# Kernel tuning notes

Measured on AMD Instinct MI355X. Metric: run time of the kernel, lower is better.

Reference implementation:

```python
import jax, jax.numpy as jnp
import numpy as np

V = 32000; DM = 512; DS = 64; K = 4; INNER = 2048; KK = 3
B = 4; N = 512; LOOPS = 6; H_CYCLES = 2; POWER = 2


def _ln(x, g, b, eps=1e-5):
    mu = jnp.mean(x, -1, keepdims=True)
    var = jnp.mean(jnp.square(x - mu), -1, keepdims=True)
    return (x - mu) * jax.lax.rsqrt(var + eps) * g + b


def _sn(W, u):
    # torch spectral_norm: one power iteration (no grad through u,v), sigma differentiable through W
    v = W.T @ u
    v = v / (jnp.linalg.norm(v) + 1e-12)
    u2 = W @ v
    u2 = u2 / (jnp.linalg.norm(u2) + 1e-12)
    u2 = jax.lax.stop_gradient(u2)
    v = jax.lax.stop_gradient(v)
    sigma = u2 @ (W @ v)
    return W / sigma


def _block(Q_in, p):
    Qn = _ln(Q_in, p['g1'], p['b1'])                       # [B,N,d]
    qp = Qn.mean(1)                                        # [B,d]
    Wq = _sn(p['hqW'], p['uq'])
    Wk = _sn(p['hkW'], p['uk'])
    Oq = (qp @ Wq.T).reshape(-1, DM, DS)                   # [B,d,D]
    Ok = (qp @ Wk.T).reshape(-1, DM, DS)
    Pq = jax.nn.elu(jnp.einsum('bnd,bde->bne', Qn, Oq) + p['BQ']) + 1.0
    Pk = jax.nn.elu(jnp.einsum('bnd,bde->bne', Qn, Ok) + p['BK']) + 1.0
    Wm = jnp.maximum(jnp.einsum('bne,bme->bnm', Pq, Pk), 0.0) ** POWER  # [B,N,N]
    Att = jnp.einsum('bnm,bmd->bnd', Wm, Qn)
    Nrm = jnp.abs(Wm.sum(-1)) + 1.0                        # [B,N]
    m = Att / Nrm[..., None] - Qn
    mp = m @ p['mW'].T + p['mb']
    Qi = Q_in + jax.nn.softplus(p['dt']) * mp
    Qn2 = _ln(Qi, p['g2'], p['b2'])
    GU = Qn2 @ p['WupW'].T                                 # [B,N,2*inner]
    G, U = GU[..., :INNER], GU[..., INNER:]
    H = jax.nn.silu(G) * U
    Ht = jnp.transpose(H, (0, 2, 1))                       # [B,inner,N]
    Hc = jax.lax.conv_general_dilated(Ht, p['convW'], (1,), [(1, 1)],
                                      dimension_numbers=('NCH', 'OIH', 'NCH'),
                                      feature_group_count=INNER)
    Hc = jnp.transpose(Hc, (0, 2, 1))
    return Qi + Hc @ p['WdownW'].T


def _run(Q, bp):
    for i in range(K):
        Q = _block(Q, {k: v[i] for k, v in bp.items()})
    return Q


def setup_inputs() -> dict:
    key = jax.random.key(0)
    ks = iter(jax.random.split(key, 48))
    nrm = lambda s, std=0.02: jax.random.normal(next(ks), s, jnp.float32) * std
    inp = {}
    inp['inputs'] = jax.random.randint(next(ks), (B, N), 0, V, jnp.int32)
    inp['labels'] = jax.random.randint(next(ks), (B, N), 0, V, jnp.int32)
    inp['halted'] = jnp.ones((B,), bool)
    inp['steps'] = jnp.zeros((B,), jnp.int32)
    inp['carry_hidden'] = jnp.zeros((B, N, DM), jnp.float32)
    inp['carry_inputs'] = jnp.zeros((B, N), jnp.int32)
    inp['carry_labels'] = jnp.zeros((B, N), jnp.int32)
    inp['embedding'] = nrm((V, DM))
    inp['pos_emb'] = nrm((8192, DM))
    inp['in_g'] = jnp.ones((DM,), jnp.float32)
    inp['in_b'] = jnp.zeros((DM,), jnp.float32)
    inp['init_hidden'] = nrm((DM,))
    inp['dt'] = jnp.full((K,), 0.1, jnp.float32)
    inp['mW'] = nrm((K, DM, DM))
    inp['mb'] = jnp.zeros((K, DM), jnp.float32)
    inp['hqW'] = nrm((K, DM * DS, DM))
    inp['hkW'] = nrm((K, DM * DS, DM))
    uq = jax.random.normal(next(ks), (K, DM * DS), jnp.float32)
    uk = jax.random.normal(next(ks), (K, DM * DS), jnp.float32)
    inp['uq'] = uq / jnp.linalg.norm(uq, axis=-1, keepdims=True)
    inp['uk'] = uk / jnp.linalg.norm(uk, axis=-1, keepdims=True)
    inp['BQ'] = nrm((K, DS))
    inp['BK'] = nrm((K, DS))
    inp['g1'] = jnp.ones((K, DM), jnp.float32)
    inp['b1'] = jnp.zeros((K, DM), jnp.float32)
    inp['g2'] = jnp.ones((K, DM), jnp.float32)
    inp['b2'] = jnp.zeros((K, DM), jnp.float32)
    inp['WupW'] = nrm((K, 2 * INNER, DM))
    inp['convW'] = nrm((K, INNER, 1, KK))
    inp['WdownW'] = nrm((K, DM, INNER))
    inp['fin_g'] = jnp.ones((DM,), jnp.float32)
    inp['fin_b'] = jnp.zeros((DM,), jnp.float32)
    inp['halt_W'] = nrm((1, DM))
    inp['halt_b'] = jnp.full((1,), -5.0, jnp.float32)
    inp['lm_head'] = nrm((V, DM))
    return inp


def reference(inputs, labels, halted, steps, carry_hidden, carry_inputs, carry_labels,
              embedding, pos_emb, in_g, in_b, init_hidden, dt, mW, mb, hqW, hkW, uq, uk,
              BQ, BK, g1, b1, g2, b2, WupW, convW, WdownW, fin_g, fin_b, halt_W, halt_b, lm_head):
    bp = dict(dt=dt, mW=mW, mb=mb, hqW=hqW, hkW=hkW, uq=uq, uk=uk, BQ=BQ, BK=BK,
              g1=g1, b1=b1, g2=g2, b2=b2, WupW=WupW, convW=convW, WdownW=WdownW)
    new_hidden = jnp.where(halted[:, None, None], init_hidden, carry_hidden)
    new_steps = jnp.where(halted, jnp.zeros_like(steps), steps)
    new_inputs = jnp.where(halted[:, None], inputs, carry_inputs)
    X = _ln(embedding[new_inputs] + pos_emb[:inputs.shape[1]][None], in_g, in_b)
    Q = new_hidden
    for _ in range(H_CYCLES - 1):  # no_grad burn-in
        Q = jax.lax.stop_gradient(_run(Q + X, bp))
    Q = _run(Q + X, bp)            # gradient pass (L_cycles = 1)
    Qf = _ln(Q, fin_g, fin_b)
    logits = Qf @ lm_head.T
    halt_logits = Qf.mean(1) @ halt_W.T + halt_b
    new_steps = new_steps + 1
    new_halted = new_steps >= LOOPS
    return logits, halt_logits, jax.lax.stop_gradient(Q), new_steps, new_halted
```

## Files before the change

### kernel.cpp

```cpp
#include <hip/hip_runtime.h>
#include <stdint.h>

#define DMD 512
#define NSEQ 512
#define NBATCH 4
#define WROWS 32768
#define VOCAB 32000

#define OFF_HALT   65536000L
#define OFF_Q      65536004L
#define OFF_STEPS  66584580L
#define OFF_HALTED 66584584L

typedef __attribute__((ext_vector_type(8))) short short8v;
typedef __attribute__((ext_vector_type(4))) float f32x4;

__device__ __forceinline__ ushort f2bf(float f){
  uint u = __builtin_bit_cast(uint, f);
  u += 0x7fffu + ((u >> 16) & 1u);
  return (ushort)(u >> 16);
}
__device__ __forceinline__ float bf2f(ushort h){
  return __builtin_bit_cast(float, (uint)h << 16);
}

__device__ __forceinline__ float block_reduce_sum256(float v, float* red){
  int t = threadIdx.x;
  red[t] = v; __syncthreads();
  for (int o = 128; o; o >>= 1){
    if (t < o) red[t] += red[t+o];
    __syncthreads();
  }
  float r = red[0]; __syncthreads();
  return r;
}

template<int MODE, int TR, int QP, int HALT>
__global__ __launch_bounds__(512) void k_ln1(
    const float* in, float* QaW, const float* X,
    const int* halted32, const float* ih, const float* ch,
    ushort* __restrict__ outb, ushort* __restrict__ outT,
    float* __restrict__ qp_part,
    const float* __restrict__ g, const float* __restrict__ b,
    const float* __restrict__ hW, float* __restrict__ hpart)
{
  __shared__ ushort lt[TR ? 16 : 1][TR ? 520 : 1];
  __shared__ float red[QP ? 4096 : 1];
  const int bb = blockIdx.y, rg = blockIdx.x;
  const int n0 = rg*16;
  const int tid = threadIdx.x, wave = tid >> 6, lane = tid & 63;
  const int c8 = lane*8;
  float qacc[8] = {};
  #pragma unroll
  for (int rr = 0; rr < 2; rr++){
    const int n = n0 + wave*2 + rr;
    const long rowo = (long)bb*262144 + (long)n*512;
    float x[8];
    if (MODE == 1){
      bool hall = (halted32[0] != 0);
      #pragma unroll
      for (int i = 0; i < 8; i++){
        float base = hall ? ih[c8+i] : ch[rowo + c8 + i];
        x[i] = base + X[rowo + c8 + i];
      }
      #pragma unroll
      for (int i = 0; i < 8; i++) QaW[rowo + c8 + i] = x[i];
    } else if (MODE == 2){
      #pragma unroll
      for (int i = 0; i < 8; i++) x[i] = in[rowo + c8 + i] + X[rowo + c8 + i];
      #pragma unroll
      for (int i = 0; i < 8; i++) QaW[rowo + c8 + i] = x[i];
    } else {
      float4 a0 = *(const float4*)(in + rowo + c8);
      float4 a1 = *(const float4*)(in + rowo + c8 + 4);
      x[0]=a0.x; x[1]=a0.y; x[2]=a0.z; x[3]=a0.w;
      x[4]=a1.x; x[5]=a1.y; x[6]=a1.z; x[7]=a1.w;
    }
    float s = 0.f, sq = 0.f;
    #pragma unroll
    for (int i = 0; i < 8; i++){ s += x[i]; sq += x[i]*x[i]; }
    #pragma unroll
    for (int m = 32; m; m >>= 1){
      s  += __shfl_xor(s, m);
      sq += __shfl_xor(sq, m);
    }
    float mu = s*(1.f/512.f);
    float var = sq*(1.f/512.f) - mu*mu;
    float rs = rsqrtf(var + 1e-5f);
    float hd = 0.f;
    short8v ov;
    #pragma unroll
    for (int i = 0; i < 8; i++){
      float o = (x[i]-mu)*rs*g[c8+i] + b[c8+i];
      ov[i] = (short)f2bf(o);
      if (QP) qacc[i] += o;
      if (HALT) hd += o * hW[c8+i];
    }
    *(short8v*)&outb[rowo + c8] = ov;
    if (TR) *(short8v*)&lt[n & 15][c8] = ov;
    if (HALT){
      #pragma unroll
      for (int m = 32; m; m >>= 1) hd += __shfl_xor(hd, m);
      if (lane == 0) atomicAdd(&hpart[bb], hd);
    }
  }
  if (QP){
    #pragma unroll
    for (int i = 0; i < 8; i++) red[wave*512 + c8 + i] = qacc[i];
    __syncthreads();
    if (wave == 0){
      #pragma unroll
      for (int i = 0; i < 8; i++){
        int c = c8 + i;
        float s = 0.f;
        #pragma unroll
        for (int w = 0; w < 8; w++) s += red[w*512 + c];
        qp_part[((long)bb*32 + rg)*512 + c] = s;
      }
    }
  }
  if (TR){
    __syncthreads();
    #pragma unroll 4
    for (int p = 0; p < 16; p++){
      int d = p*32 + (tid >> 4);
      int n = tid & 15;
      outT[(long)bb*262144 + (long)d*512 + n0 + n] = lt[n][d];
    }
  }
}

__global__ void k_embed_ln(const int* __restrict__ inputs, const int* __restrict__ cinputs,
                           const int* __restrict__ halted32,
                           const float* __restrict__ emb, const float* __restrict__ pos,
                           const float* __restrict__ g, const float* __restrict__ b,
                           float* __restrict__ X){
  __shared__ float red[256];
  int r = blockIdx.x; int t = threadIdx.x;
  int n = r & 511;
  bool hall = (halted32[0] != 0);
  int tok = hall ? inputs[r] : cinputs[r];
  const float* e = emb + (long)tok*DMD;
  const float* p = pos + (long)n*DMD;
  float v0 = e[t]+p[t], v1 = e[t+256]+p[t+256];
  float mu = block_reduce_sum256(v0+v1, red) * (1.f/DMD);
  float d0 = v0-mu, d1 = v1-mu;
  float var = block_reduce_sum256(d0*d0+d1*d1, red) * (1.f/DMD);
  float rs = rsqrtf(var + 1e-5f);
  X[(long)r*DMD+t]     = d0*rs*g[t]     + b[t];
  X[(long)r*DMD+t+256] = d1*rs*g[t+256] + b[t+256];
}

__global__ __launch_bounds__(512) void k_sn_v(
    const float* __restrict__ hqW, const float* __restrict__ hkW,
    const float* __restrict__ uq, const float* __restrict__ uk,
    float* __restrict__ vpart, ushort* __restrict__ Wbf){
  __shared__ float red[8*520];
  int z = blockIdx.y; int k = z >> 1, qk = z & 1;
  const float* W = (qk ? hkW : hqW) + (long)k*WROWS*DMD;
  const float* u = (qk ? uk : uq) + (long)k*WROWS;
  ushort* Wb = Wbf ? (Wbf + (long)z*WROWS*DMD) : nullptr;
  int t = threadIdx.x;
  int c8 = (t & 63) * 8;
  int rsub = t >> 6;
  int r0 = blockIdx.x * 256;
  float acc[8] = {};
  for (int r = rsub; r < 256; r += 16){
    int ra = r0 + r, rb = r0 + r + 8;
    long offa = (long)ra*DMD + c8, offb = (long)rb*DMD + c8;
    float4 a0 = *(const float4*)(W + offa);
    float4 a1 = *(const float4*)(W + offa + 4);
    float4 b0 = *(const float4*)(W + offb);
    float4 b1 = *(const float4*)(W + offb + 4);
    float ua = u[ra], ub = u[rb];
    float av[8] = {a0.x,a0.y,a0.z,a0.w,a1.x,a1.y,a1.z,a1.w};
    float bv[8] = {b0.x,b0.y,b0.z,b0.w,b1.x,b1.y,b1.z,b1.w};
    #pragma unroll
    for (int i = 0; i < 8; i++) acc[i] += av[i]*ua + bv[i]*ub;
    if (Wb){
      short8v oa, ob;
      #pragma unroll
      for (int i = 0; i < 8; i++){ oa[i] = (short)f2bf(av[i]); ob[i] = (short)f2bf(bv[i]); }
      long ca = (long)((ra & 63)*512 + (ra >> 6));
      long cb = (long)((rb & 63)*512 + (rb >> 6));
      *(short8v*)(Wb + ca*DMD + c8) = oa;
      *(short8v*)(Wb + cb*DMD + c8) = ob;
    }
  }
  #pragma unroll
  for (int i = 0; i < 8; i++) red[rsub*520 + c8 + i] = acc[i];
  __syncthreads();
  if (rsub == 0){
    #pragma unroll
    for (int i = 0; i < 8; i++){
      int c = c8 + i;
      float s = 0.f;
      #pragma unroll
      for (int w = 0; w < 8; w++) s += red[w*520 + c];
      vpart[((long)z*128 + blockIdx.x)*512 + c] = s;
    }
  }
}

__global__ __launch_bounds__(512) void k_sn_norm(const float* __restrict__ vpart,
                                                 float* __restrict__ vraw,
                                                 ushort* __restrict__ qpb){
  __shared__ float red[512];
  int z = blockIdx.x; int t = threadIdx.x;
  float s = 0.f;
  for (int c = 0; c < 128; c++) s += vpart[((long)z*128 + c)*512 + t];
  red[t] = s*s; __syncthreads();
  for (int o = 256; o; o >>= 1){
    if (t < o) red[t] += red[t+o];
    __syncthreads();
  }
  float nrm = sqrtf(red[0]);
  float v = s / (nrm + 1e-12f);
  vraw[z*512 + t] = v;
  ushort* p = qpb + (long)z*32768;
  p[4*512 + t] = f2bf(v);
  for (int r = 5; r < 64; r++) p[r*512 + t] = 0;
}

__global__ void k_sn_s(const float* __restrict__ hqW, const float* __restrict__ hkW,
                       const float* __restrict__ vraw, float* __restrict__ ssqp){
  int z = blockIdx.y; int k = z >> 1, qk = z & 1;
  const float* W = (qk ? hkW : hqW) + (long)k*WROWS*DMD;
  const float* v = vraw + z*DMD;
  int wave = threadIdx.x >> 6, lane = threadIdx.x & 63;
  float vreg[8];
  #pragma unroll
  for (int i = 0; i < 8; i++) vreg[i] = v[lane + 64*i];
  int r0 = blockIdx.x*256 + wave*64;
  float acc = 0.f;
  for (int r = r0; r < r0+64; r++){
    float p = 0.f;
    #pragma unroll
    for (int i = 0; i < 8; i++)
      p += W[(long)r*DMD + lane + 64*i] * vreg[i];
    for (int off = 32; off; off >>= 1) p += __shfl_down(p, off);
    if (lane == 0) acc += p*p;
  }
  if (lane == 0) atomicAdd(&ssqp[z*64 + (blockIdx.x & 63)], acc);
}

__global__ void k_proj(const float* __restrict__ hqW, const float* __restrict__ hkW,
                       const float* __restrict__ qp,
                       ushort* __restrict__ OqT, ushort* __restrict__ OkT, int k){
  int z = blockIdx.y;
  const float* W = (z ? hkW : hqW) + (long)k*WROWS*DMD;
  ushort* O = z ? OkT : OqT;
  int wave = threadIdx.x >> 6, lane = threadIdx.x & 63;
  long r = (long)blockIdx.x*4 + wave;
  float a0=0,a1=0,a2=0,a3=0;
  for (int j = lane; j < DMD; j += 64){
    float w = W[r*DMD + j];
    a0 += w*qp[j]; a1 += w*qp[DMD+j]; a2 += w*qp[2*DMD+j]; a3 += w*qp[3*DMD+j];
  }
  for (int off = 32; off; off >>= 1){
    a0 += __shfl_down(a0,off); a1 += __shfl_down(a1,off);
    a2 += __shfl_down(a2,off); a3 += __shfl_down(a3,off);
  }
  if (lane == 0){
    int d = (int)(r >> 6), e = (int)(r & 63);
    long o = (long)e*512 + d;
    O[o] = f2bf(a0); O[32768+o] = f2bf(a1);
    O[2*32768+o] = f2bf(a2); O[3*32768+o] = f2bf(a3);
  }
}

template<int BM, int BN, int WM, int WN, int EPI, int BFOUT, int DUAL, int RSUM>
__global__ __launch_bounds__(256) void mm_bt(
    const ushort* __restrict__ A, const ushort* __restrict__ B, void* __restrict__ C,
    int N, int K, long sA, long sB, long sC,
    const float* __restrict__ bias, const float* __restrict__ bias2,
    const float* __restrict__ res, const ushort* __restrict__ resb,
    const float* __restrict__ dtp, int dtidx,
    float* __restrict__ aux, const float* __restrict__ ssqp)
{
  __shared__ ushort As[BM*64];
  __shared__ ushort Bs[BN*64];
  const int z = blockIdx.z;
  const float* biasz = bias;
  if (DUAL){
    A += (long)(z & 3)*sA;
    if (z >= 4) biasz = bias2;
  } else {
    A += (long)z*sA;
  }
  B += (long)z*sB;
  const int tm = blockIdx.y*BM, tn = DUAL ? 0 : blockIdx.x*BN;
  const int tid = threadIdx.x;
  const int wid = tid >> 6, lane = tid & 63;
  constexpr int NWN = BN/WN;
  const int wr = wid / NWN, wc = wid % NWN;
  constexpr int FM = WM/16, FN = WN/16;
  const int ln15 = lane & 15, kq = lane >> 4;
  constexpr int LA = BM/32;
  constexpr int LB = BN/32;
  f32x4 acc[FM][FN] = {};

  for (int k0 = 0; k0 < K; k0 += 64){
    #pragma unroll
    for (int l = 0; l < LA; l++){
      int slot = tid + l*256;
      int row = slot >> 3, ch = slot & 7;
      int gch = ch ^ (row & 7);
      const char* g = (const char*)(A + (long)(tm+row)*K + k0) + gch*16;
      ushort* lp = As + (size_t)(wid*64 + l*256)*8;
      __builtin_amdgcn_global_load_lds((const __attribute__((address_space(1))) void*)g,
                                       (__attribute__((address_space(3))) void*)lp, 16, 0, 0);
    }
    #pragma unroll
    for (int l = 0; l < LB; l++){
      int slot = tid + l*256;
      int row = slot >> 3, ch = slot & 7;
      int gch = ch ^ (row & 7);
      const char* g = (const char*)(B + (long)(tn+row)*K + k0) + gch*16;
      ushort* lp = Bs + (size_t)(wid*64 + l*256)*8;
      __builtin_amdgcn_global_load_lds((const __attribute__((address_space(1))) void*)g,
                                       (__attribute__((address_space(3))) void*)lp, 16, 0, 0);
    }
    __syncthreads();
    #pragma unroll
    for (int ks = 0; ks < 2; ks++){
      short8v af[FM], bfr[FN];
      #pragma unroll
      for (int i = 0; i < FM; i++){
        int row = wr*WM + i*16 + ln15;
        af[i] = *(const short8v*)&As[row*64 + (((ks*4+kq) ^ (row&7))*8)];
      }
      #pragma unroll
      for (int j = 0; j < FN; j++){
        int row = wc*WN + j*16 + ln15;
        bfr[j] = *(const short8v*)&Bs[row*64 + (((ks*4+kq) ^ (row&7))*8)];
      }
      #pragma unroll
      for (int i = 0; i < FM; i++)
        #pragma unroll
        for (int j = 0; j < FN; j++)
          acc[i][j] = __builtin_amdgcn_mfma_f32_16x16x32_bf16(af[i], bfr[j], acc[i][j], 0, 0, 0);
    }
    __syncthreads();
  }

  float sp = 0.f, invs = 1.f;
  if (EPI == 3) sp = log1pf(expf(dtp[dtidx]));
  if (EPI == 1){
    const float* sq = ssqp + (DUAL ? (z >> 2)*64 : 0);
    float s2 = 0.f;
    for (int i = 0; i < 64; i++) s2 += sq[i];
    invs = (sqrtf(s2) + 1e-12f) / s2;
  }
  float* Cf = (float*)C + (long)z*sC;
  ushort* Cb = (ushort*)C + (long)z*sC;
  const float* rz = res ? (res + (long)z*sC) : nullptr;
  const ushort* rzb = resb ? (resb + (long)z*sC) : nullptr;
  const float* nrmz = (EPI == 5) ? (bias + (long)z*512) : nullptr;
  float rsv[FM][4] = {};
  float sacc = 0.f;
  #pragma unroll
  for (int i = 0; i < FM; i++){
    int row0 = tm + wr*WM + i*16 + kq*4;
    #pragma unroll
    for (int j = 0; j < FN; j++){
      int col = tn + wc*WN + j*16 + ln15;
      #pragma unroll
      for (int r = 0; r < 4; r++){
        int row = row0 + r;
        long idx = (long)row*N + col;
        float v = acc[i][j][r];
        if (EPI == 6){
          if (row < 4) Cb[idx] = f2bf(v);
          else if (row == 4) sacc += v*v;
          continue;
        }
        if (EPI == 1){ v = v*invs + biasz[col]; v = v > 0.f ? v : expm1f(v); v += 1.f; }
        else if (EPI == 2){ v = fmaxf(v, 0.f); v = v*v; if (RSUM) rsv[i][r] += v; }
        else if (EPI == 3){ v = rz[idx] + sp*(v + biasz[col]); }
        else if (EPI == 4){ v = v + rz[idx]; if (aux) aux[idx] = v; }
        else if (EPI == 5){ v = v/(fabsf(nrmz[row])+1.f) - bf2f(rzb[idx]); }
        if (BFOUT) Cb[idx] = f2bf(v);
        else       Cf[idx] = v;
      }
    }
  }
  if (EPI == 6){
    if (aux){
      sacc += __shfl_xor(sacc, 1); sacc += __shfl_xor(sacc, 2);
      sacc += __shfl_xor(sacc, 4); sacc += __shfl_xor(sacc, 8);
      if (wr == 0 && kq == 1 && ln15 == 0)
        atomicAdd(&aux[(long)z*64 + ((int)blockIdx.x & 63)], sacc);
    }
    return;
  }
  if (RSUM && EPI == 2){
    #pragma unroll
    for (int i = 0; i < FM; i++){
      #pragma unroll
      for (int r = 0; r < 4; r++){
        float x = rsv[i][r];
        x += __shfl_xor(x, 1); x += __shfl_xor(x, 2);
        x += __shfl_xor(x, 4); x += __shfl_xor(x, 8);
        if (ln15 == 0)
          atomicAdd(&aux[(long)z*512 + tm + wr*WM + i*16 + kq*4 + r], x);
      }
    }
  }
}

__global__ void k_qp2(const float* __restrict__ part, float* __restrict__ qp,
                      ushort* __restrict__ qpb, float* __restrict__ nrm_raw){
  int b = blockIdx.x, t = threadIdx.x;
  float s = 0.f;
  #pragma unroll
  for (int c = 0; c < 32; c++) s += part[((long)b*32 + c)*512 + t];
  float val = s * (1.f/512.f);
  qp[b*512 + t] = val;
  ushort bv = f2bf(val);
  #pragma unroll
  for (int z = 0; z < 8; z++)
    qpb[(long)z*32768 + (long)b*512 + t] = bv;
  nrm_raw[b*512 + t] = 0.f;
}

__global__ void k_convfuse(const ushort* __restrict__ GU, const float* __restrict__ w,
                           ushort* __restrict__ Hc){
  int r = blockIdx.x;
  int n = r & 511;
  int c = threadIdx.x * 8;
  long base = (long)r*4096 + c;
  float o[8] = {};
  if (n > 0){
    short8v gv = *(const short8v*)&GU[base-4096];
    short8v uv = *(const short8v*)&GU[base-4096+2048];
    #pragma unroll
    for (int i = 0; i < 8; i++){
      float g = bf2f((ushort)gv[i]), u = bf2f((ushort)uv[i]);
      o[i] += g/(1.f+expf(-g))*u * w[(c+i)*3+0];
    }
  }
  {
    short8v gv = *(const short8v*)&GU[base];
    short8v uv = *(const short8v*)&GU[base+2048];
    #pragma unroll
    for (int i = 0; i < 8; i++){
      float g = bf2f((ushort)gv[i]), u = bf2f((ushort)uv[i]);
      o[i] += g/(1.f+expf(-g))*u * w[(c+i)*3+1];
    }
  }
  if (n < 511){
    short8v gv = *(const short8v*)&GU[base+4096];
    short8v uv = *(const short8v*)&GU[base+4096+2048];
    #pragma unroll
    for (int i = 0; i < 8; i++){
      float g = bf2f((ushort)gv[i]), u = bf2f((ushort)uv[i]);
      o[i] += g/(1.f+expf(-g))*u * w[(c+i)*3+2];
    }
  }
  short8v ov;
  #pragma unroll
  for (int i = 0; i < 8; i++) ov[i] = (short)f2bf(o[i]);
  *(short8v*)&Hc[(long)r*2048 + c] = ov;
}

__global__ void k_cvt3(const float* __restrict__ s0, ushort* __restrict__ d0, long n0,
                       const float* __restrict__ s1, ushort* __restrict__ d1, long n1,
                       const float* __restrict__ s2, ushort* __restrict__ d2, long n2){
  long i = ((long)blockIdx.x*256 + threadIdx.x)*4;
  const float* s; ushort* d; long off;
  if (i < n0){ s = s0; d = d0; off = i; }
  else if (i < n0 + n1){ s = s1; d = d1; off = i - n0; }
  else { s = s2; d = d2; off = i - n0 - n1; }
  float4 v = *(const float4*)(s + off);
  ushort4 o;
  o.x = f2bf(v.x); o.y = f2bf(v.y); o.z = f2bf(v.z); o.w = f2bf(v.w);
  *(ushort4*)(d + off) = o;
}

__global__ void k_cvt(const float* __restrict__ in, ushort* __restrict__ out){
  long i = ((long)blockIdx.x*256 + threadIdx.x)*4;
  float4 v = *(const float4*)(in + i);
  ushort4 o;
  o.x = f2bf(v.x); o.y = f2bf(v.y); o.z = f2bf(v.z); o.w = f2bf(v.w);
  *(ushort4*)(out + i) = o;
}

__global__ void k_fin(const int* __restrict__ halted32, const int* __restrict__ steps,
                      const float* __restrict__ hpart, const float* __restrict__ hb,
                      float* __restrict__ o_halt, float* __restrict__ o_steps,
                      float* __restrict__ o_halted){
  int t = threadIdx.x;
  if (t < NBATCH){
    o_halt[t] = hpart[t]*(1.f/512.f) + hb[0];
    bool hall = (halted32[0] != 0);
    int ns = (hall ? 0 : steps[t]) + 1;
    o_steps[t] = (float)ns;
    o_halted[t] = ns >= 6 ? 1.f : 0.f;
  }
}

extern "C" void kernel_launch(void* const* d_in, const int* in_sizes, int n_in,
                              void* d_out, int out_size, void* d_ws, size_t ws_size,
                              hipStream_t stream)
{
  const int*     inputs       = (const int*)d_in[0];
  const int*     halted32     = (const int*)d_in[2];
  const int*     steps        = (const int*)d_in[3];
  const float*   carry_hidden = (const float*)d_in[4];
  const int*     carry_inputs = (const int*)d_in[5];
  const float*   embedding    = (const float*)d_in[7];
  const float*   pos_emb      = (const float*)d_in[8];
  const float*   in_g = (const float*)d_in[9];
  const float*   in_b = (const float*)d_in[10];
  const float*   init_hidden = (const float*)d_in[11];
  const float*   dt   = (const float*)d_in[12];
  const float*   mW   = (const float*)d_in[13];
  const float*   mb   = (const float*)d_in[14];
  const float*   hqW  = (const float*)d_in[15];
  const float*   hkW  = (const float*)d_in[16];
  const float*   uq   = (const float*)d_in[17];
  const float*   uk   = (const float*)d_in[18];
  const float*   BQb  = (const float*)d_in[19];
  const float*   BKb  = (const float*)d_in[20];
  const float*   g1   = (const float*)d_in[21];
  const float*   b1   = (const float*)d_in[22];
  const float*   g2   = (const float*)d_in[23];
  const float*   b2   = (const float*)d_in[24];
  const float*   WupW = (const float*)d_in[25];
  const float*   convW= (const float*)d_in[26];
  const float*   WdownW=(const float*)d_in[27];
  const float*   fin_g= (const float*)d_in[28];
  const float*   fin_b= (const float*)d_in[29];
  const float*   halt_W=(const float*)d_in[30];
  const float*   halt_b=(const float*)d_in[31];
  const float*   lm_head=(const float*)d_in[32];
  float* out = (float*)d_out;

  float* ws = (float*)d_ws;
  float*  X    = ws;
  float*  Qa   = ws +  1048576;
  float*  Qb   = ws +  2097152;
  ushort* qpb  = (ushort*)(ws + 3145728);
  float*  vpart  = ws + 3276800;
  float*  qp_part= ws + 3801088;
  ushort* GU_bf  = (ushort*)(ws +  4194304);
  ushort* Hc_bf  = (ushort*)(ws +  8388608);
  ushort* m_bf   = (ushort*)(ws + 10485760);
  ushort* Wm_bf  = (ushort*)(ws + 11010048);
  ushort* QnT_bf = (ushort*)(ws + 11534336);
  ushort* Pq_bf  = (ushort*)(ws + 12058624);
  ushort* OqT    = (ushort*)(ws + 12189696);
  ushort* lm_bf  = (ushort*)(ws +  4194304);
  ushort* Qn_bf  = (ushort*)(ws + 13369344);
  ushort* mW_bf  = (ushort*)(ws + 13893632);
  ushort* Wup_bf = (ushort*)(ws + 14417920);
  ushort* Wdn_bf = (ushort*)(ws + 18612224);
  float*  qp       = ws + 20709376;
  float*  Nrm_raw  = ws + 20711424;
  float*  vraw     = ws + 20713472;
  float*  ssq_part = ws + 20717568;
  float*  hpart    = ws + 20718080;
  ushort* W_bf = (ushort*)(ws + 20750976);
  const size_t NEED_BF = (size_t)(20750976 + 67108864) * 4;
  const bool useBf = ws_size >= NEED_BF;

  k_cvt3<<<13312, 256, 0, stream>>>(mW, mW_bf, 1048576L,
                                    WupW, Wup_bf, 8388608L,
                                    WdownW, Wdn_bf, 4194304L);

  hipMemsetAsync(ssq_part, 0, 576*sizeof(float), stream);
  k_sn_v<<<dim3(128,8), 512, 0, stream>>>(hqW, hkW, uq, uk, vpart,
                                          useBf ? W_bf : nullptr);
  k_sn_norm<<<8, 512, 0, stream>>>(vpart, vraw, qpb);
  if (!useBf)
    k_sn_s<<<dim3(128,8), 256, 0, stream>>>(hqW, hkW, vraw, ssq_part);

  k_embed_ln<<<2048, 256, 0, stream>>>(inputs, carry_inputs, halted32,
                                       embedding, pos_emb, in_g, in_b, X);

  for (int cyc = 0; cyc < 2; cyc++){
    for (int k = 0; k < 4; k++){
      if (k == 0){
        if (cyc == 0)
          k_ln1<1,1,1,0><<<dim3(32,4), 512, 0, stream>>>(
              Qa, Qa, X, halted32, init_hidden, carry_hidden,
              Qn_bf, QnT_bf, qp_part, g1 + k*DMD, b1 + k*DMD, nullptr, nullptr);
        else
          k_ln1<2,1,1,0><<<dim3(32,4), 512, 0, stream>>>(
              Qa, Qa, X, nullptr, nullptr, nullptr,
              Qn_bf, QnT_bf, qp_part, g1 + k*DMD, b1 + k*DMD, nullptr, nullptr);
      } else {
        k_ln1<0,1,1,0><<<dim3(32,4), 512, 0, stream>>>(
            Qa, nullptr, nullptr, nullptr, nullptr, nullptr,
            Qn_bf, QnT_bf, qp_part, g1 + k*DMD, b1 + k*DMD, nullptr, nullptr);
      }
      k_qp2<<<4, 512, 0, stream>>>(qp_part, qp, qpb, Nrm_raw);
      if (useBf)
        mm_bt<64,64,32,32,6,1,0,1><<<dim3(512,1,2), 256, 0, stream>>>(
            qpb + (long)k*2*32768, W_bf + (long)k*2*16777216, OqT,
            32768, 512, 32768, 16777216, 131072,
            nullptr, nullptr, nullptr, nullptr, nullptr, 0,
            (cyc == 0) ? (ssq_part + k*128) : nullptr, nullptr);
      else
        k_proj<<<dim3(8192,2), 256, 0, stream>>>(hqW, hkW, qp, OqT, OqT + 131072, k);
      mm_bt<64,64,32,32,1,1,1,0><<<dim3(1,8,8), 256, 0, stream>>>(
          Qn_bf, OqT, Pq_bf, 64, 512, 262144, 32768, 32768,
          BQb + k*64, BKb + k*64, nullptr, nullptr, nullptr, 0,
          nullptr, ssq_part + k*128);
      mm_bt<64,64,32,32,2,1,0,1><<<dim3(8,8,4), 256, 0, stream>>>(
          Pq_bf, Pq_bf + 131072, Wm_bf, 512, 64, 32768, 32768, 262144,
          nullptr, nullptr, nullptr, nullptr, nullptr, 0, Nrm_raw, nullptr);
      mm_bt<64,64,32,32,5,1,0,0><<<dim3(8,8,4), 256, 0, stream>>>(
          Wm_bf, QnT_bf, m_bf, 512, 512, 262144, 262144, 262144,
          Nrm_raw, nullptr, nullptr, Qn_bf, nullptr, 0, nullptr, nullptr);
      mm_bt<64,64,32,32,3,0,0,0><<<dim3(8,32,1), 256, 0, stream>>>(
          m_bf, mW_bf + (long)k*262144, Qb, 512, 512, 0, 0, 0,
          mb + k*DMD, nullptr, Qa, nullptr, dt, k, nullptr, nullptr);
      k_ln1<0,0,0,0><<<dim3(32,4), 512, 0, stream>>>(
          Qb, nullptr, nullptr, nullptr, nullptr, nullptr,
          Qn_bf, nullptr, nullptr, g2 + k*DMD, b2 + k*DMD, nullptr, nullptr);
      mm_bt<128,128,64,64,0,1,0,0><<<dim3(32,16,1), 256, 0, stream>>>(
          Qn_bf, Wup_bf + (long)k*2097152, GU_bf, 4096, 512, 0, 0, 0,
          nullptr, nullptr, nullptr, nullptr, nullptr, 0, nullptr, nullptr);
      k_convfuse<<<2048, 256, 0, stream>>>(GU_bf, convW + (long)k*2048*3, Hc_bf);
      float* aux = (cyc == 1 && k == 3) ? (out + OFF_Q) : nullptr;
      mm_bt<64,64,32,32,4,0,0,0><<<dim3(8,32,1), 256, 0, stream>>>(
          Hc_bf, Wdn_bf + (long)k*1048576, Qa, 512, 2048, 0, 0, 0,
          nullptr, nullptr, Qb, nullptr, nullptr, 0, aux, nullptr);
    }
  }

  k_ln1<0,0,0,1><<<dim3(32,4), 512, 0, stream>>>(
      Qa, nullptr, nullptr, nullptr, nullptr, nullptr,
      Qn_bf, nullptr, nullptr, fin_g, fin_b, halt_W, hpart);
  k_cvt<<<16000, 256, 0, stream>>>(lm_head, lm_bf);
  mm_bt<128,128,64,64,0,0,0,0><<<dim3(250,16,1), 256, 0, stream>>>(
      Qn_bf, lm_bf, out, 32000, 512, 0, 0, 0,
      nullptr, nullptr, nullptr, nullptr, nullptr, 0, nullptr, nullptr);
  k_fin<<<1, 64, 0, stream>>>(halted32, steps, hpart, halt_b,
                              out + OFF_HALT, out + OFF_STEPS, out + OFF_HALTED);
}
```

Before: 1.546 ms.

## Fuse attention score and value matmuls; convert lm_head to bf16 inside GEMM loads

Adds a k_attn kernel that computes the squared-ReLU scores Pq·Pkᵀ tile by tile in LDS, accumulates the row normalizers locally, and immediately multiplies each score tile by Qn. This removes the [B,N,N] Wm buffer round-trip, the Nrm atomics and their zeroing, and one launch per block. Separately, the lm_head GEMM now reads fp32 weights and converts them to bf16 while staging into LDS, replacing the standalone k_cvt pass. The attention kernel recomputes scores once per 64-column output group (8 groups), and the fused conversion gives up the async global_load_lds path for B.

```diff
diff --git a/kernel.cpp b/kernel.cpp
--- a/kernel.cpp
+++ b/kernel.cpp
@@ -269,7 +269,7 @@
   }
 }
 
-template<int BM, int BN, int WM, int WN, int EPI, int BFOUT, int DUAL, int RSUM>
+template<int BM, int BN, int WM, int WN, int EPI, int BFOUT, int DUAL, int RSUM, int CVTB = 0>
 __global__ __launch_bounds__(256) void mm_bt(
     const ushort* __restrict__ A, const ushort* __restrict__ B, void* __restrict__ C,
     int N, int K, long sA, long sB, long sC,
@@ -288,7 +288,7 @@
   } else {
     A += (long)z*sA;
   }
-  B += (long)z*sB;
+  if (!CVTB) B += (long)z*sB;
   const int tm = blockIdx.y*BM, tn = DUAL ? 0 : blockIdx.x*BN;
   const int tid = threadIdx.x;
   const int wid = tid >> 6, lane = tid & 63;
@@ -316,10 +316,22 @@
       int slot = tid + l*256;
       int row = slot >> 3, ch = slot & 7;
       int gch = ch ^ (row & 7);
-      const char* g = (const char*)(B + (long)(tn+row)*K + k0) + gch*16;
-      ushort* lp = Bs + (size_t)(wid*64 + l*256)*8;
-      __builtin_amdgcn_global_load_lds((const __attribute__((address_space(1))) void*)g,
-                                       (__attribute__((address_space(3))) void*)lp, 16, 0, 0);
+      if (CVTB){
+        const float* Bf = (const float*)B;
+        const float* src = Bf + (long)(tn+row)*K + k0 + gch*8;
+        float4 v0 = *(const float4*)src;
+        float4 v1 = *(const float4*)(src + 4);
+        float vv[8] = {v0.x,v0.y,v0.z,v0.w,v1.x,v1.y,v1.z,v1.w};
+        short8v o;
+        #pragma unroll
+        for (int i = 0; i < 8; i++) o[i] = (short)f2bf(vv[i]);
+        *(short8v*)&Bs[(size_t)slot*8] = o;
+      } else {
+        const char* g = (const char*)(B + (long)(tn+row)*K + k0) + gch*16;
+        ushort* lp = Bs + (size_t)(wid*64 + l*256)*8;
+        __builtin_amdgcn_global_load_lds((const __attribute__((address_space(1))) void*)g,
+                                         (__attribute__((address_space(3))) void*)lp, 16, 0, 0);
+      }
     }
     __syncthreads();
     #pragma unroll
@@ -355,9 +367,6 @@
   float* Cf = (float*)C + (long)z*sC;
   ushort* Cb = (ushort*)C + (long)z*sC;
   const float* rz = res ? (res + (long)z*sC) : nullptr;
-  const ushort* rzb = resb ? (resb + (long)z*sC) : nullptr;
-  const float* nrmz = (EPI == 5) ? (bias + (long)z*512) : nullptr;
-  float rsv[FM][4] = {};
   float sacc = 0.f;
   #pragma unroll
   for (int i = 0; i < FM; i++){
@@ -376,41 +385,152 @@
           continue;
         }
         if (EPI == 1){ v = v*invs + biasz[col]; v = v > 0.f ? v : expm1f(v); v += 1.f; }
-        else if (EPI == 2){ v = fmaxf(v, 0.f); v = v*v; if (RSUM) rsv[i][r] += v; }
         else if (EPI == 3){ v = rz[idx] + sp*(v + biasz[col]); }
         else if (EPI == 4){ v = v + rz[idx]; if (aux) aux[idx] = v; }
-        else if (EPI == 5){ v = v/(fabsf(nrmz[row])+1.f) - bf2f(rzb[idx]); }
         if (BFOUT) Cb[idx] = f2bf(v);
         else       Cf[idx] = v;
       }
     }
   }
-  if (EPI == 6){
-    if (aux){
-      sacc += __shfl_xor(sacc, 1); sacc += __shfl_xor(sacc, 2);
-      sacc += __shfl_xor(sacc, 4); sacc += __shfl_xor(sacc, 8);
-      if (wr == 0 && kq == 1 && ln15 == 0)
-        atomicAdd(&aux[(long)z*64 + ((int)blockIdx.x & 63)], sacc);
-    }
-    return;
-  }
-  if (RSUM && EPI == 2){
-    #pragma unroll
-    for (int i = 0; i < FM; i++){
+  if (EPI == 6 && aux){
+    sacc += __shfl_xor(sacc, 1); sacc += __shfl_xor(sacc, 2);
+    sacc += __shfl_xor(sacc, 4); sacc += __shfl_xor(sacc, 8);
+    if (wr == 0 && kq == 1 && ln15 == 0)
+      atomicAdd(&aux[(long)z*64 + ((int)blockIdx.x & 63)], sacc);
+  }
+}
+
+__global__ __launch_bounds__(256) void k_attn(
+    const ushort* __restrict__ Pqk, const ushort* __restrict__ QnT,
+    const ushort* __restrict__ Qn, ushort* __restrict__ m_out)
+{
+  __shared__ ushort Aq[64*64];
+  __shared__ ushort Bk[64*64];
+  __shared__ ushort Qs[64*64];
+  __shared__ ushort Ws[64*72];
+  __shared__ float nrmL[2][64];
+  const int cg = blockIdx.x, nt = blockIdx.y, b = blockIdx.z;
+  const int tid = threadIdx.x, wid = tid >> 6;
+  const int lane = tid & 63, ln15 = lane & 15, kq = lane >> 4;
+  const int wr = wid >> 1, wc = wid & 1;
+  const ushort* Pq  = Pqk + (long)b*32768 + (long)nt*4096;
+  const ushort* Pk0 = Pqk + 131072 + (long)b*32768;
+  const ushort* Qt  = QnT + (long)b*262144 + (long)(cg*64)*512;
+
+  #pragma unroll
+  for (int l = 0; l < 2; l++){
+    int slot = tid + l*256;
+    int row = slot >> 3, gch = (slot & 7) ^ (row & 7);
+    __builtin_amdgcn_global_load_lds(
+        (const __attribute__((address_space(1))) void*)((const char*)(Pq + (long)row*64) + gch*16),
+        (__attribute__((address_space(3))) void*)(Aq + (size_t)(wid*64 + l*256)*8), 16, 0, 0);
+  }
+  f32x4 acc[2][2] = {};
+  float nacc[2][4] = {};
+  for (int mt = 0; mt < 8; mt++){
+    #pragma unroll
+    for (int l = 0; l < 2; l++){
+      int slot = tid + l*256;
+      int row = slot >> 3, gch = (slot & 7) ^ (row & 7);
+      __builtin_amdgcn_global_load_lds(
+          (const __attribute__((address_space(1))) void*)((const char*)(Pk0 + (long)mt*4096 + (long)row*64) + gch*16),
+          (__attribute__((address_space(3))) void*)(Bk + (size_t)(wid*64 + l*256)*8), 16, 0, 0);
+      __builtin_amdgcn_global_load_lds(
+          (const __attribute__((address_space(1))) void*)((const char*)(Qt + (long)row*512 + mt*64) + gch*16),
+          (__attribute__((address_space(3))) void*)(Qs + (size_t)(wid*64 + l*256)*8), 16, 0, 0);
+    }
+    __syncthreads();
+    f32x4 sA[2][2] = {};
+    #pragma unroll
+    for (int ks = 0; ks < 2; ks++){
+      short8v af[2], bfr[2];
+      #pragma unroll
+      for (int i = 0; i < 2; i++){
+        int row = wr*32 + i*16 + ln15;
+        af[i] = *(const short8v*)&Aq[row*64 + (((ks*4+kq) ^ (row&7))*8)];
+      }
+      #pragma unroll
+      for (int j = 0; j < 2; j++){
+        int row = wc*32 + j*16 + ln15;
+        bfr[j] = *(const short8v*)&Bk[row*64 + (((ks*4+kq) ^ (row&7))*8)];
+      }
+      #pragma unroll
+      for (int i = 0; i < 2; i++)
+        #pragma unroll
+        for (int j = 0; j < 2; j++)
+          sA[i][j] = __builtin_amdgcn_mfma_f32_16x16x32_bf16(af[i], bfr[j], sA[i][j], 0, 0, 0);
+    }
+    float t[2][4] = {};
+    #pragma unroll
+    for (int i = 0; i < 2; i++)
+      #pragma unroll
+      for (int j = 0; j < 2; j++)
+        #pragma unroll
+        for (int r = 0; r < 4; r++){
+          float v = fmaxf(sA[i][j][r], 0.f); v = v*v;
+          t[i][r] += v;
+          int row = wr*32 + i*16 + kq*4 + r;
+          int col = wc*32 + j*16 + ln15;
+          Ws[row*72 + col] = f2bf(v);
+        }
+    #pragma unroll
+    for (int i = 0; i < 2; i++)
       #pragma unroll
       for (int r = 0; r < 4; r++){
-        float x = rsv[i][r];
+        float x = t[i][r];
         x += __shfl_xor(x, 1); x += __shfl_xor(x, 2);
         x += __shfl_xor(x, 4); x += __shfl_xor(x, 8);
-        if (ln15 == 0)
-          atomicAdd(&aux[(long)z*512 + tm + wr*WM + i*16 + kq*4 + r], x);
+        nacc[i][r] += x;
+      }
+    __syncthreads();
+    #pragma unroll
+    for (int ks = 0; ks < 2; ks++){
+      short8v af[2], bfr[2];
+      #pragma unroll
+      for (int i = 0; i < 2; i++){
+        int row = wr*32 + i*16 + ln15;
+        af[i] = *(const short8v*)&Ws[row*72 + (ks*4+kq)*8];
+      }
+      #pragma unroll
+      for (int j = 0; j < 2; j++){
+        int row = wc*32 + j*16 + ln15;
+        bfr[j] = *(const short8v*)&Qs[row*64 + (((ks*4+kq) ^ (row&7))*8)];
+      }
+      #pragma unroll
+      for (int i = 0; i < 2; i++)
+        #pragma unroll
+        for (int j = 0; j < 2; j++)
+          acc[i][j] = __builtin_amdgcn_mfma_f32_16x16x32_bf16(af[i], bfr[j], acc[i][j], 0, 0, 0);
+    }
+    __syncthreads();
+  }
+  if (ln15 == 0){
+    #pragma unroll
+    for (int i = 0; i < 2; i++)
+      #pragma unroll
+      for (int r = 0; r < 4; r++)
+        nrmL[wc][wr*32 + i*16 + kq*4 + r] = nacc[i][r];
+  }
+  __syncthreads();
+  #pragma unroll
+  for (int i = 0; i < 2; i++){
+    #pragma unroll
+    for (int r = 0; r < 4; r++){
+      int rowl = wr*32 + i*16 + kq*4 + r;
+      float Nr = fabsf(nrmL[0][rowl] + nrmL[1][rowl]) + 1.f;
+      int n = nt*64 + rowl;
+      #pragma unroll
+      for (int j = 0; j < 2; j++){
+        int col = cg*64 + wc*32 + j*16 + ln15;
+        long idx = (long)b*262144 + (long)n*512 + col;
+        m_out[idx] = f2bf(acc[i][j][r]/Nr - bf2f(Qn[idx]));
       }
     }
   }
 }
 
 __global__ void k_qp2(const float* __restrict__ part, float* __restrict__ qp,
-                      ushort* __restrict__ qpb, float* __restrict__ nrm_raw){
+                      ushort* __restrict__ qpb){
   int b = blockIdx.x, t = threadIdx.x;
   float s = 0.f;
   #pragma unroll
@@ -421,7 +541,6 @@
   #pragma unroll
   for (int z = 0; z < 8; z++)
     qpb[(long)z*32768 + (long)b*512 + t] = bv;
-  nrm_raw[b*512 + t] = 0.f;
 }
 
 __global__ void k_convfuse(const ushort* __restrict__ GU, const float* __restrict__ w,
@@ -476,14 +595,6 @@
   ushort4 o;
   o.x = f2bf(v.x); o.y = f2bf(v.y); o.z = f2bf(v.z); o.w = f2bf(v.w);
   *(ushort4*)(d + off) = o;
-}
-
-__global__ void k_cvt(const float* __restrict__ in, ushort* __restrict__ out){
-  long i = ((long)blockIdx.x*256 + threadIdx.x)*4;
-  float4 v = *(const float4*)(in + i);
-  ushort4 o;
-  o.x = f2bf(v.x); o.y = f2bf(v.y); o.z = f2bf(v.z); o.w = f2bf(v.w);
-  *(ushort4*)(out + i) = o;
 }
 
 __global__ void k_fin(const int* __restrict__ halted32, const int* __restrict__ steps,
@@ -547,17 +658,14 @@
   ushort* GU_bf  = (ushort*)(ws +  4194304);
   ushort* Hc_bf  = (ushort*)(ws +  8388608);
   ushort* m_bf   = (ushort*)(ws + 10485760);
-  ushort* Wm_bf  = (ushort*)(ws + 11010048);
   ushort* QnT_bf = (ushort*)(ws + 11534336);
   ushort* Pq_bf  = (ushort*)(ws + 12058624);
   ushort* OqT    = (ushort*)(ws + 12189696);
-  ushort* lm_bf  = (ushort*)(ws +  4194304);
   ushort* Qn_bf  = (ushort*)(ws + 13369344);
   ushort* mW_bf  = (ushort*)(ws + 13893632);
   ushort* Wup_bf = (ushort*)(ws + 14417920);
   ushort* Wdn_bf = (ushort*)(ws + 18612224);
   float*  qp       = ws + 20709376;
-  float*  Nrm_raw  = ws + 20711424;
   float*  vraw     = ws + 20713472;
   float*  ssq_part = ws + 20717568;
   float*  hpart    = ws + 20718080;
@@ -595,7 +703,7 @@
             Qa, nullptr, nullptr, nullptr, nullptr, nullptr,
             Qn_bf, QnT_bf, qp_part, g1 + k*DMD, b1 + k*DMD, nullptr, nullptr);
       }
-      k_qp2<<<4, 512, 0, stream>>>(qp_part, qp, qpb, Nrm_raw);
+      k_qp2<<<4, 512, 0, stream>>>(qp_part, qp, qpb);
       if (useBf)
         mm_bt<64,64,32,32,6,1,0,1><<<dim3(512,1,2), 256, 0, stream>>>(
             qpb + (long)k*2*32768, W_bf + (long)k*2*16777216, OqT,
@@ -608,12 +716,7 @@
           Qn_bf, OqT, Pq_bf, 64, 512, 262144, 32768, 32768,
           BQb + k*64, BKb + k*64, nullptr, nullptr, nullptr, 0,
           nullptr, ssq_part + k*128);
-      mm_bt<64,64,32,32,2,1,0,1><<<dim3(8,8,4), 256, 0, stream>>>(
-          Pq_bf, Pq_bf + 131072, Wm_bf, 512, 64, 32768, 32768, 262144,
-          nullptr, nullptr, nullptr, nullptr, nullptr, 0, Nrm_raw, nullptr);
-      mm_bt<64,64,32,32,5,1,0,0><<<dim3(8,8,4), 256, 0, stream>>>(
-          Wm_bf, QnT_bf, m_bf, 512, 512, 262144, 262144, 262144,
-          Nrm_raw, nullptr, nullptr, Qn_bf, nullptr, 0, nullptr, nullptr);
+      k_attn<<<dim3(8,8,4), 256, 0, stream>>>(Pq_bf, QnT_bf, Qn_bf, m_bf);
       mm_bt<64,64,32,32,3,0,0,0><<<dim3(8,32,1), 256, 0, stream>>>(
           m_bf, mW_bf + (long)k*262144, Qb, 512, 512, 0, 0, 0,
           mb + k*DMD, nullptr, Qa, nullptr, dt, k, nullptr, nullptr);
@@ -634,9 +737,8 @@
   k_ln1<0,0,0,1><<<dim3(32,4), 512, 0, stream>>>(
       Qa, nullptr, nullptr, nullptr, nullptr, nullptr,
       Qn_bf, nullptr, nullptr, fin_g, fin_b, halt_W, hpart);
-  k_cvt<<<16000, 256, 0, stream>>>(lm_head, lm_bf);
-  mm_bt<128,128,64,64,0,0,0,0><<<dim3(250,16,1), 256, 0, stream>>>(
-      Qn_bf, lm_bf, out, 32000, 512, 0, 0, 0,
+  mm_bt<128,128,64,64,0,0,0,0,1><<<dim3(250,16,1), 256, 0, stream>>>(
+      Qn_bf, (const ushort*)lm_head, out, 32000, 512, 0, 0, 0,
       nullptr, nullptr, nullptr, nullptr, nullptr, 0, nullptr, nullptr);
   k_fin<<<1, 64, 0, stream>>>(halted32, steps, hpart, halt_b,
                               out + OFF_HALT, out + OFF_STEPS, out + OFF_HALTED);
```

Measured after the change: 1.623 ms. 5.0% more time.
